# Kernel tuning notes

Hardware: AMD Instinct MI355X
Metric: run time of the kernel (lower is better)

## Reference

```python
import jax, jax.numpy as jnp
import numpy as np

EPS = 1e-5

def avg_pool3s2(x):
    # AvgPool2d(kernel=3, stride=2, no padding) on NCHW
    s = jax.lax.reduce_window(x, 0.0, jax.lax.add, (1, 1, 3, 3), (1, 1, 2, 2), 'VALID')
    return s / 9.0

def conv1x1(x, W):
    # x: [n,c,h,w], W: [out,c]
    return jnp.einsum('nchw,oc->nohw', x, W)

def batchnorm(x, g, b):
    # training-mode BN over (N,H,W), biased variance (matches torch normalization)
    m = x.mean(axis=(0, 2, 3), keepdims=True)
    v = x.var(axis=(0, 2, 3), keepdims=True)
    return (x - m) * jax.lax.rsqrt(v + EPS) * g[None, :, None, None] + b[None, :, None, None]

def coord_features(hp, wp):
    # [8, hp, wp]: xmin, ymin, xmax, ymax, xctr, yctr, 1/W, 1/H
    w = jnp.arange(wp, dtype=jnp.float32)
    h = jnp.arange(hp, dtype=jnp.float32)
    xmin = w / wp * 2 - 1
    xmax = (w + 1) / wp * 2 - 1
    xctr = (xmin + xmax) / 2
    ymin = h / hp * 2 - 1
    ymax = (h + 1) / hp * 2 - 1
    yctr = (ymin + ymax) / 2
    bx = lambda a: jnp.broadcast_to(a[None, :], (hp, wp))
    by = lambda a: jnp.broadcast_to(a[:, None], (hp, wp))
    const = lambda v: jnp.full((hp, wp), v, dtype=jnp.float32)
    return jnp.stack([bx(xmin), by(ymin), bx(xmax), by(ymax), bx(xctr), by(yctr),
                      const(1.0 / wp), const(1.0 / hp)], axis=0)

def resize_bilinear_ac(x, H, W):
    # bilinear upsample with align_corners=True, x: [n,c,h,w]
    h, w = x.shape[2], x.shape[3]
    ys = jnp.linspace(0.0, h - 1.0, H)
    xs = jnp.linspace(0.0, w - 1.0, W)
    y0 = jnp.floor(ys).astype(jnp.int32); y1 = jnp.minimum(y0 + 1, h - 1); wy = (ys - y0)[None, None, :, None]
    x0 = jnp.floor(xs).astype(jnp.int32); x1 = jnp.minimum(x0 + 1, w - 1); wx = (xs - x0)[None, None, None, :]
    rows = x[:, :, y0, :] * (1 - wy) + x[:, :, y1, :] * wy          # [n,c,H,w]
    return rows[:, :, :, x0] * (1 - wx) + rows[:, :, :, x1] * wx    # [n,c,H,W]

def setup_inputs() -> dict:
    key = jax.random.key(0)
    ks = jax.random.split(key, 8)
    n, in_dim, hid, h, w = 4, 256, 10, 129, 129
    d = hid + 8  # 18
    return {
        'p_fea': jax.random.normal(ks[0], (n, in_dim, h, w), dtype=jnp.float32),
        'hu': jax.random.normal(ks[1], (n, hid, h, w), dtype=jnp.float32),
        'Wq': jax.random.normal(ks[2], (d, d), dtype=jnp.float32) * 0.05,
        'Wk': jax.random.normal(ks[3], (d, in_dim + 8), dtype=jnp.float32) * 0.05,
        'Wv': jax.random.normal(ks[4], (128, in_dim), dtype=jnp.float32) * 0.05,
        'g_v': jnp.ones((128,), dtype=jnp.float32),
        'b_v': jnp.zeros((128,), dtype=jnp.float32),
        'Wp': jax.random.normal(ks[5], (hid, 128), dtype=jnp.float32) * 0.05,
        'g_p': jnp.ones((hid,), dtype=jnp.float32),
        'b_p': jnp.zeros((hid,), dtype=jnp.float32),
    }

def reference(p_fea, hu, Wq, Wk, Wv, g_v, b_v, Wp, g_p, b_p):
    n, c, h, w = p_fea.shape
    p = avg_pool3s2(p_fea)   # [n,256,hp,wp]
    u = avg_pool3s2(hu)      # [n,10,hp,wp]
    hp, wp = p.shape[2], p.shape[3]
    L = hp * wp
    coord = jnp.broadcast_to(coord_features(hp, wp)[None], (n, 8, hp, wp))
    query = conv1x1(jnp.concatenate([u, coord], axis=1), Wq).reshape(n, -1, L).transpose(0, 2, 1)  # [n,L,18]
    key_t = conv1x1(jnp.concatenate([p, coord], axis=1), Wk).reshape(n, -1, L)                      # [n,18,L]
    val = jax.nn.relu(batchnorm(conv1x1(p, Wv), g_v, b_v)).reshape(n, 128, L)                       # [n,128,L]
    energy = jnp.einsum('nlc,ncm->nlm', query, key_t)            # [n,L,L]
    attn = jax.nn.softmax(energy, axis=-1)
    ctx = jnp.einsum('ncm,nlm->ncl', val, attn).reshape(n, 128, hp, wp)
    ctx = jax.nn.relu(batchnorm(conv1x1(ctx, Wp), g_p, b_p))     # [n,10,hp,wp]
    return resize_bilinear_ac(ctx, h, w)                          # [n,10,h,w]
```

## Files before the change

kernel.cpp:

```cpp
#include <hip/hip_runtime.h>
#include <hip/hip_bf16.h>
#include <cstdint>

#define NN   4
#define LL   4096
#define DD   18
#define CVV  128
#define CIN  256
#define CUU  10
#define HH   129
#define COO  10

typedef unsigned short ushort_t;
typedef __attribute__((ext_vector_type(8))) short short8v;
typedef __attribute__((ext_vector_type(4))) float f32x4;

#define P_OFF    ((size_t)0)
#define U_OFF    ((size_t)4194304)
#define VP_OFF   ((size_t)4358144)
#define QT_OFF   ((size_t)6455296)
#define KT_OFF   ((size_t)6717440)
#define VT_OFF   ((size_t)6979584)
#define VSC_OFF  ((size_t)8028160)
#define VSH_OFF  ((size_t)8028288)
#define S2_OFF   ((size_t)8028416)
#define SH2_OFF  ((size_t)8028432)
#define PART_OFF ((size_t)8028448)
#define ML_OFF   ((size_t)8030496)

static __device__ __forceinline__ ushort_t f2bf(float x) {
    unsigned int u = __float_as_uint(x);
    unsigned int r = (u + 0x7fffu + ((u >> 16) & 1u)) >> 16;
    return (ushort_t)r;
}

static __device__ __forceinline__ void gload16(const void* g, void* l) {
    __builtin_amdgcn_global_load_lds(
        (const __attribute__((address_space(1))) void*)g,
        (__attribute__((address_space(3))) void*)l, 16, 0, 0);
}

__global__ __launch_bounds__(256) void pool2_kernel(const float* __restrict__ src,
                                                    float* __restrict__ dst) {
    int b = blockIdx.x;
    int plane = b >> 4;
    int rg = b & 15;
    __shared__ float rows[9][132];
    const float* sp = src + (size_t)plane * (HH * HH) + (size_t)(rg * 8) * HH;
    #pragma unroll
    for (int j = 0; j < 9; ++j) {
        if (threadIdx.x < HH) rows[j][threadIdx.x] = sp[(size_t)j * HH + threadIdx.x];
    }
    __syncthreads();
    int row = threadIdx.x >> 6, ow = threadIdx.x & 63;
    const float* r0 = rows[2 * row];
    const float* r1 = rows[2 * row + 1];
    const float* r2 = rows[2 * row + 2];
    int x = 2 * ow;
    float sum = r0[x] + r0[x + 1] + r0[x + 2]
              + r1[x] + r1[x + 1] + r1[x + 2]
              + r2[x] + r2[x + 1] + r2[x + 2];
    dst[(size_t)plane * 4096 + (size_t)(rg * 4 + row) * 64 + ow] = sum * (1.0f / 9.0f);
}

__global__ __launch_bounds__(256) void qk2_kernel(const float* __restrict__ p,
                                                  const float* __restrict__ u,
                                                  const float* __restrict__ Wq,
                                                  const float* __restrict__ Wk,
                                                  ushort_t* __restrict__ qt,
                                                  char* __restrict__ kt_c) {
    int n = blockIdx.x >> 6;
    int mb = blockIdx.x & 63;
    int tid = threadIdx.x;
    int mloc = tid & 63;
    int cs = tid >> 6;
    int m = mb * 64 + mloc;
    int hi = m >> 6, wi = m & 63;

    __shared__ float kacc[4][64][21];

    float coord[8];
    coord[0] = wi * (2.0f / 64.0f) - 1.0f;
    coord[1] = hi * (2.0f / 64.0f) - 1.0f;
    coord[2] = (wi + 1) * (2.0f / 64.0f) - 1.0f;
    coord[3] = (hi + 1) * (2.0f / 64.0f) - 1.0f;
    coord[4] = 0.5f * (coord[0] + coord[2]);
    coord[5] = 0.5f * (coord[1] + coord[3]);
    coord[6] = 1.0f / 64.0f;
    coord[7] = 1.0f / 64.0f;

    {
        float acc[DD];
        #pragma unroll
        for (int o = 0; o < DD; ++o) acc[o] = 0.0f;
        const float* pc = p + ((size_t)(n * CIN + cs * 64)) * LL + m;
        for (int c0 = 0; c0 < 64; ++c0) {
            float pv = pc[(size_t)c0 * LL];
            const float* wr = Wk + (cs * 64 + c0);
            #pragma unroll
            for (int o = 0; o < DD; ++o) acc[o] = fmaf(pv, wr[o * 264], acc[o]);
        }
        if (cs == 3) {
            #pragma unroll
            for (int j = 0; j < 8; ++j) {
                float cv = coord[j];
                #pragma unroll
                for (int o = 0; o < DD; ++o) acc[o] = fmaf(cv, Wk[o * 264 + CIN + j], acc[o]);
            }
        }
        #pragma unroll
        for (int o = 0; o < DD; ++o) kacc[cs][mloc][o] = acc[o];
    }
    if (cs == 0) {
        float acc[DD];
        #pragma unroll
        for (int o = 0; o < DD; ++o) acc[o] = 0.0f;
        for (int cq = 0; cq < CUU; ++cq) {
            float uv = u[((size_t)(n * CUU + cq)) * LL + m];
            #pragma unroll
            for (int o = 0; o < DD; ++o) acc[o] = fmaf(uv, Wq[o * DD + cq], acc[o]);
        }
        #pragma unroll
        for (int j = 0; j < 8; ++j) {
            float cv = coord[j];
            #pragma unroll
            for (int o = 0; o < DD; ++o) acc[o] = fmaf(cv, Wq[o * DD + CUU + j], acc[o]);
        }
        union { short8v v[4]; ushort_t s[32]; } pk;
        #pragma unroll
        for (int o = 0; o < 32; ++o) pk.s[o] = (o < DD) ? f2bf(acc[o]) : (ushort_t)0;
        short8v* qrow = (short8v*)(qt + ((size_t)(n * LL) + m) * 32);
        #pragma unroll
        for (int j = 0; j < 4; ++j) qrow[j] = pk.v[j];
    }
    __syncthreads();
    {
        int j = cs;
        union { short8v v; ushort_t s[8]; } pk;
        #pragma unroll
        for (int i = 0; i < 8; ++i) {
            int o = j * 8 + i;
            float v = 0.0f;
            if (o < DD)
                v = kacc[0][mloc][o] + kacc[1][mloc][o] + kacc[2][mloc][o] + kacc[3][mloc][o];
            pk.s[i] = (o < DD) ? f2bf(v) : (ushort_t)0;
        }
        int byte = ((mloc << 6) | (j << 4)) ^ (((mloc >> 1) & 7) << 4);
        *(short8v*)(kt_c + (size_t)n * 262144 + (size_t)mb * 4096 + byte) = pk.v;
    }
}

__global__ __launch_bounds__(256, 2) void val_gemm2_kernel(const float* __restrict__ p,
                                                           const float* __restrict__ Wv,
                                                           float* __restrict__ val_pre) {
    int b = blockIdx.x;
    int n  = b >> 7;
    int cb = (b >> 5) & 3;
    int mb = b & 31;
    int tid = threadIdx.x;
    int cg = tid >> 5;
    int mg = tid & 31;
    int ch0 = cb * 32;
    int m0 = mb * 128;

    __shared__ float Wt[256][36];

    {
        int c4 = tid & 63;
        int chq = tid >> 6;
        #pragma unroll
        for (int j = 0; j < 8; ++j) {
            int ch = chq * 8 + j;
            float4 v = *(const float4*)&Wv[(size_t)(ch0 + ch) * CIN + c4 * 4];
            Wt[c4 * 4 + 0][ch] = v.x;
            Wt[c4 * 4 + 1][ch] = v.y;
            Wt[c4 * 4 + 2][ch] = v.z;
            Wt[c4 * 4 + 3][ch] = v.w;
        }
    }
    __syncthreads();

    const float* pb = p + (size_t)n * CIN * LL + m0 + mg * 4;
    f32x4 a0 = {0.f,0.f,0.f,0.f}, a1 = {0.f,0.f,0.f,0.f};
    f32x4 a2 = {0.f,0.f,0.f,0.f}, a3 = {0.f,0.f,0.f,0.f};

    #pragma unroll 4
    for (int c = 0; c < CIN; ++c) {
        f32x4 pv = *(const f32x4*)(pb + (size_t)c * LL);
        f32x4 wv = *(const f32x4*)&Wt[c][cg * 4];
        a0 += pv * wv.x;
        a1 += pv * wv.y;
        a2 += pv * wv.z;
        a3 += pv * wv.w;
    }

    size_t out = ((size_t)(n * CVV + ch0 + cg * 4)) * LL + m0 + mg * 4;
    *(f32x4*)&val_pre[out]           = a0;
    *(f32x4*)&val_pre[out + LL]      = a1;
    *(f32x4*)&val_pre[out + 2 * LL]  = a2;
    *(f32x4*)&val_pre[out + 3 * LL]  = a3;
}

__global__ __launch_bounds__(256) void bn_partial_kernel(const float* __restrict__ src,
                                                         float* __restrict__ part, int C) {
    int ch = blockIdx.x >> 3;
    int s = blockIdx.x & 7;
    float s1 = 0.0f, s2 = 0.0f;
    #pragma unroll
    for (int k = 0; k < 8; ++k) {
        int e = s * 2048 + k * 256 + threadIdx.x;
        int n = e >> 12;
        int m = e & 4095;
        float v = src[((size_t)(n * C + ch)) * LL + m];
        s1 += v;
        s2 = fmaf(v, v, s2);
    }
    __shared__ float rs[4], rs2[4];
    #pragma unroll
    for (int off = 32; off; off >>= 1) {
        s1 += __shfl_down(s1, off);
        s2 += __shfl_down(s2, off);
    }
    int wid = threadIdx.x >> 6;
    if ((threadIdx.x & 63) == 0) { rs[wid] = s1; rs2[wid] = s2; }
    __syncthreads();
    if (threadIdx.x == 0) {
        part[(size_t)blockIdx.x * 2]     = rs[0] + rs[1] + rs[2] + rs[3];
        part[(size_t)blockIdx.x * 2 + 1] = rs2[0] + rs2[1] + rs2[2] + rs2[3];
    }
}

__global__ __launch_bounds__(128) void bn_finalize_kernel(const float* __restrict__ part,
                                                          const float* __restrict__ g,
                                                          const float* __restrict__ bta,
                                                          float* __restrict__ scale,
                                                          float* __restrict__ shift, int C) {
    int ch = threadIdx.x;
    if (ch >= C) return;
    float s1 = 0.0f, s2 = 0.0f;
    #pragma unroll
    for (int s = 0; s < 8; ++s) {
        s1 += part[(size_t)(ch * 8 + s) * 2];
        s2 += part[(size_t)(ch * 8 + s) * 2 + 1];
    }
    float mean = s1 * (1.0f / (NN * LL));
    float var = s2 * (1.0f / (NN * LL)) - mean * mean;
    float inv = rsqrtf(var + 1e-5f);
    float sc = g[ch] * inv;
    scale[ch] = sc;
    shift[ch] = bta[ch] - mean * sc;
}

__global__ __launch_bounds__(256) void bn_apply_kernel(const float* __restrict__ val_pre,
                                                       const float* __restrict__ scale,
                                                       const float* __restrict__ shift,
                                                       char* __restrict__ vt_c) {
    int t = blockIdx.x * 256 + threadIdx.x;
    int m = t & 4095;
    int ch = (t >> 12) & 127;
    int n = t >> 19;
    float v = val_pre[((size_t)(n * CVV + ch)) * LL + m];
    v = fmaf(v, scale[ch], shift[ch]);
    ushort_t r = f2bf(fmaxf(v, 0.0f));
    int tile = m >> 6, mloc = m & 63;
    size_t byte = (size_t)n * 1048576 + (size_t)tile * 16384
                + (size_t)(((ch << 7) | (mloc << 1)) ^ ((ch & 7) << 4));
    *(ushort_t*)(vt_c + byte) = r;
}

struct PW { union { ushort_t p[16][72]; float ot[16][20]; }; };

__global__ __launch_bounds__(256, 2) void attn_flash_kernel(const ushort_t* __restrict__ qt,
                                                            const char* __restrict__ kt_c,
                                                            const char* __restrict__ vt_c,
                                                            float* __restrict__ Op,
                                                            float* __restrict__ Mp,
                                                            float* __restrict__ Lp) {
    int orig = blockIdx.x;
    int bid = ((orig & 7) << 6) | (orig >> 3);
    int qb = bid & 63;
    int sM = (bid >> 6) & 1;
    int n = bid >> 7;
    int tid = threadIdx.x;
    int w = tid >> 6, lane = tid & 63, c = lane & 15, g = lane >> 4;
    int l0w = qb * 64 + w * 16;

    __shared__ __align__(16) ushort_t K_t[2][2048];
    __shared__ __align__(16) ushort_t V_t[2][8192];
    __shared__ PW pws[4];

    const char* ktb = kt_c + (size_t)n * 262144;
    const char* vtb = vt_c + (size_t)n * 1048576;
    int tk64 = sM * 32;

    short8v qf = *(const short8v*)(qt + (((size_t)n * LL + l0w + c) << 5) + g * 8);
    int vxor = (c & 7) << 4;

    float M[4] = {-3.0e38f, -3.0e38f, -3.0e38f, -3.0e38f};
    {
        const char* src = ktb + (size_t)tk64 * 4096 + w * 2048 + lane * 16;
        gload16(src, (char*)V_t[0] + w * 2048);
        gload16(src + 1024, (char*)V_t[0] + w * 2048 + 1024);
    }
    __syncthreads();
    int buf = 0;
    for (int mt = 0; mt < 16; ++mt) {
        if (mt + 1 < 16) {
            const char* src = ktb + (size_t)(tk64 + (mt + 1) * 2) * 4096 + w * 2048 + lane * 16;
            gload16(src, (char*)V_t[buf ^ 1] + w * 2048);
            gload16(src + 1024, (char*)V_t[buf ^ 1] + w * 2048 + 1024);
        }
        const char* kb = (const char*)V_t[buf];
        #pragma unroll
        for (int t = 0; t < 8; ++t) {
            int krow = t * 16 + c;
            int kby = ((krow << 6) | (g << 4)) ^ (((krow >> 1) & 7) << 4);
            short8v kf = *(const short8v*)(kb + kby);
            f32x4 S = __builtin_amdgcn_mfma_f32_16x16x32_bf16(qf, kf, (f32x4){0.f, 0.f, 0.f, 0.f}, 0, 0, 0);
            #pragma unroll
            for (int r = 0; r < 4; ++r) M[r] = fmaxf(M[r], S[r]);
        }
        __syncthreads();
        buf ^= 1;
    }
    #pragma unroll
    for (int off = 1; off < 16; off <<= 1) {
        #pragma unroll
        for (int r = 0; r < 4; ++r) M[r] = fmaxf(M[r], __shfl_xor(M[r], off));
    }

    f32x4 O[8];
    #pragma unroll
    for (int i = 0; i < 8; ++i) O[i] = (f32x4){0.f, 0.f, 0.f, 0.f};
    float Lacc[4] = {0.f, 0.f, 0.f, 0.f};

    {
        const char* ks = ktb + (size_t)tk64 * 4096 + w * 1024 + lane * 16;
        gload16(ks, (char*)K_t[0] + w * 1024);
        const char* vs = vtb + (size_t)tk64 * 16384 + w * 4096 + lane * 16;
        #pragma unroll
        for (int i = 0; i < 4; ++i)
            gload16(vs + i * 1024, (char*)V_t[0] + w * 4096 + i * 1024);
    }
    __syncthreads();
    buf = 0;
    for (int mt = 0; mt < 32; ++mt) {
        if (mt + 1 < 32) {
            const char* ks = ktb + (size_t)(tk64 + mt + 1) * 4096 + w * 1024 + lane * 16;
            gload16(ks, (char*)K_t[buf ^ 1] + w * 1024);
            const char* vs = vtb + (size_t)(tk64 + mt + 1) * 16384 + w * 4096 + lane * 16;
            #pragma unroll
            for (int i = 0; i < 4; ++i)
                gload16(vs + i * 1024, (char*)V_t[buf ^ 1] + w * 4096 + i * 1024);
        }
        f32x4 S[4];
        const char* kb = (const char*)K_t[buf];
        #pragma unroll
        for (int t = 0; t < 4; ++t) {
            int krow = t * 16 + c;
            int kby = ((krow << 6) | (g << 4)) ^ (((krow >> 1) & 7) << 4);
            short8v kf = *(const short8v*)(kb + kby);
            S[t] = __builtin_amdgcn_mfma_f32_16x16x32_bf16(qf, kf, (f32x4){0.f, 0.f, 0.f, 0.f}, 0, 0, 0);
        }
        #pragma unroll
        for (int t = 0; t < 4; ++t) {
            #pragma unroll
            for (int r = 0; r < 4; ++r) {
                float pv = __expf(S[t][r] - M[r]);
                Lacc[r] += pv;
                pws[w].p[g * 4 + r][t * 16 + c] = f2bf(pv);
            }
        }
        short8v pa0 = *(const short8v*)&pws[w].p[c][g * 8];
        short8v pa1 = *(const short8v*)&pws[w].p[c][32 + g * 8];
        const char* vb = (const char*)V_t[buf];
        #pragma unroll
        for (int ct = 0; ct < 8; ++ct) {
            int row = ct * 16 + c;
            int vby0 = (row << 7) | ((g << 4) ^ vxor);
            int vby1 = (row << 7) | (((1 << 6) | (g << 4)) ^ vxor);
            short8v v0 = *(const short8v*)(vb + vby0);
            short8v v1 = *(const short8v*)(vb + vby1);
            O[ct] = __builtin_amdgcn_mfma_f32_16x16x32_bf16(pa0, v0, O[ct], 0, 0, 0);
            O[ct] = __builtin_amdgcn_mfma_f32_16x16x32_bf16(pa1, v1, O[ct], 0, 0, 0);
        }
        __syncthreads();
        buf ^= 1;
    }
    #pragma unroll
    for (int off = 1; off < 16; off <<= 1) {
        #pragma unroll
        for (int r = 0; r < 4; ++r) Lacc[r] += __shfl_xor(Lacc[r], off);
    }

    size_t obase = ((size_t)(sM * NN + n) * LL + l0w);
    #pragma unroll
    for (int ct = 0; ct < 8; ++ct) {
        #pragma unroll
        for (int r = 0; r < 4; ++r) pws[w].ot[g * 4 + r][c] = O[ct][r];
        float4 v = *(float4*)&pws[w].ot[c][g * 4];
        *(float4*)&Op[(obase + c) * CVV + ct * 16 + g * 4] = v;
    }
    if (c == 0) {
        #pragma unroll
        for (int r = 0; r < 4; ++r) {
            Mp[sM * (NN * LL) + n * LL + l0w + g * 4 + r] = M[r];
            Lp[sM * (NN * LL) + n * LL + l0w + g * 4 + r] = Lacc[r];
        }
    }
}

__global__ __launch_bounds__(256) void proj_merge_kernel(const float* __restrict__ Op,
                                                         const float* __restrict__ Mp,
                                                         const float* __restrict__ Lp,
                                                         const float* __restrict__ Wp,
                                                         float* __restrict__ out_pre) {
    int idx = blockIdx.x * 256 + threadIdx.x;
    int n = idx >> 12;
    int l = idx & 4095;
    int nl = n * LL + l;
    float m0 = Mp[nl], m1 = Mp[NN * LL + nl];
    float l0v = Lp[nl], l1v = Lp[NN * LL + nl];
    float Ms = fmaxf(m0, m1);
    float w0 = __expf(m0 - Ms), w1 = __expf(m1 - Ms);
    float inv = 1.0f / (w0 * l0v + w1 * l1v);
    w0 *= inv; w1 *= inv;

    const float4* a4 = (const float4*)(Op + (size_t)nl * CVV);
    const float4* b4 = (const float4*)(Op + ((size_t)(NN * LL) + nl) * CVV);
    float acc[COO];
    #pragma unroll
    for (int o = 0; o < COO; ++o) acc[o] = 0.0f;
    for (int c4 = 0; c4 < CVV / 4; ++c4) {
        float4 a = a4[c4], b = b4[c4];
        float4 v;
        v.x = fmaf(w1, b.x, w0 * a.x);
        v.y = fmaf(w1, b.y, w0 * a.y);
        v.z = fmaf(w1, b.z, w0 * a.z);
        v.w = fmaf(w1, b.w, w0 * a.w);
        #pragma unroll
        for (int o = 0; o < COO; ++o) {
            const float* wr = Wp + o * CVV + c4 * 4;
            acc[o] = fmaf(v.x, wr[0], acc[o]);
            acc[o] = fmaf(v.y, wr[1], acc[o]);
            acc[o] = fmaf(v.z, wr[2], acc[o]);
            acc[o] = fmaf(v.w, wr[3], acc[o]);
        }
    }
    #pragma unroll
    for (int o = 0; o < COO; ++o)
        out_pre[((size_t)(n * COO + o)) * LL + l] = acc[o];
}

__global__ __launch_bounds__(256) void resize_kernel(const float* __restrict__ out_pre,
                                                     const float* __restrict__ scale,
                                                     const float* __restrict__ shift,
                                                     float* __restrict__ out,
                                                     int total) {
    int idx = blockIdx.x * 256 + threadIdx.x;
    if (idx >= total) return;
    int ow = idx % HH;
    int t = idx / HH;
    int oh = t % HH;
    int t2 = t / HH;
    int o = t2 % COO;
    int n = t2 / COO;

    const float r = 63.0f / 128.0f;
    float y = oh * r;
    float x = ow * r;
    int y0 = (int)y;
    int x0 = (int)x;
    float wy = y - y0;
    float wx = x - x0;
    int y1 = min(y0 + 1, 63);
    int x1 = min(x0 + 1, 63);

    const float* base = out_pre + ((size_t)(n * COO + o)) * LL;
    float sc = scale[o], sh = shift[o];
    float v00 = fmaxf(fmaf(base[y0 * 64 + x0], sc, sh), 0.0f);
    float v01 = fmaxf(fmaf(base[y0 * 64 + x1], sc, sh), 0.0f);
    float v10 = fmaxf(fmaf(base[y1 * 64 + x0], sc, sh), 0.0f);
    float v11 = fmaxf(fmaf(base[y1 * 64 + x1], sc, sh), 0.0f);
    float top = v00 * (1.0f - wx) + v01 * wx;
    float bot = v10 * (1.0f - wx) + v11 * wx;
    out[idx] = top * (1.0f - wy) + bot * wy;
}

extern "C" void kernel_launch(void* const* d_in, const int* in_sizes, int n_in,
                              void* d_out, int out_size, void* d_ws, size_t ws_size,
                              hipStream_t stream) {
    (void)in_sizes; (void)n_in; (void)out_size; (void)ws_size;
    const float* p_fea = (const float*)d_in[0];
    const float* hu    = (const float*)d_in[1];
    const float* Wq    = (const float*)d_in[2];
    const float* Wk    = (const float*)d_in[3];
    const float* Wv    = (const float*)d_in[4];
    const float* g_v   = (const float*)d_in[5];
    const float* b_v   = (const float*)d_in[6];
    const float* Wp    = (const float*)d_in[7];
    const float* g_p   = (const float*)d_in[8];
    const float* b_p   = (const float*)d_in[9];

    float* ws = (float*)d_ws;
    float*    p       = ws + P_OFF;
    float*    u       = ws + U_OFF;
    float*    val_pre = ws + VP_OFF;
    ushort_t* qtb     = (ushort_t*)(ws + QT_OFF);
    char*     ktb     = (char*)(ws + KT_OFF);
    char*     vtb     = (char*)(ws + VT_OFF);
    float*    Opart   = ws + P_OFF;
    float*    out_pre = ws + U_OFF;
    float*    vscale  = ws + VSC_OFF;
    float*    vshift  = ws + VSH_OFF;
    float*    scale2  = ws + S2_OFF;
    float*    shift2  = ws + SH2_OFF;
    float*    part    = ws + PART_OFF;
    float*    Mpart   = ws + ML_OFF;
    float*    Lpart   = ws + ML_OFF + 32768;

    pool2_kernel<<<NN * CIN * 16, 256, 0, stream>>>(p_fea, p);
    pool2_kernel<<<NN * CUU * 16, 256, 0, stream>>>(hu, u);
    qk2_kernel<<<256, 256, 0, stream>>>(p, u, Wq, Wk, qtb, ktb);
    val_gemm2_kernel<<<512, 256, 0, stream>>>(p, Wv, val_pre);
    bn_partial_kernel<<<CVV * 8, 256, 0, stream>>>(val_pre, part, CVV);
    bn_finalize_kernel<<<1, 128, 0, stream>>>(part, g_v, b_v, vscale, vshift, CVV);
    bn_apply_kernel<<<(NN * CVV * LL) / 256, 256, 0, stream>>>(val_pre, vscale, vshift, vtb);
    attn_flash_kernel<<<512, 256, 0, stream>>>(qtb, ktb, vtb, Opart, Mpart, Lpart);
    proj_merge_kernel<<<(NN * LL) / 256, 256, 0, stream>>>(Opart, Mpart, Lpart, Wp, out_pre);
    bn_partial_kernel<<<COO * 8, 256, 0, stream>>>(out_pre, part, COO);
    bn_finalize_kernel<<<1, 128, 0, stream>>>(part, g_p, b_p, scale2, shift2, COO);
    {
        int total = NN * COO * HH * HH;
        resize_kernel<<<(total + 255) / 256, 256, 0, stream>>>(out_pre, scale2, shift2,
                                                               (float*)d_out, total);
    }
}
```

Measured before the change: 155.1 us.

## Replace exact row-max pass with Cauchy-style bound from per-channel key abs maxima

Drops the first full QK^T pass in the attention kernel, which only computed exact row maxima. Instead, the qk kernel atomically records the per-batch, per-channel maximum absolute key value, and the attention kernel uses sum_i |q_i|*max|k_i| as an upper bound for the softmax max. The bound is shared across the two split halves, so the merge stays consistent. This halves the QK MFMA work and its K loads, but a loose bound risks exp underflow and lost precision. The BN partial and apply kernels are also vectorised to 8 elements per thread with float4 loads and 16-byte packed bf16 stores.

```diff
diff --git a/kernel.cpp b/kernel.cpp
--- a/kernel.cpp
+++ b/kernel.cpp
@@ -26,7 +26,7 @@
 #define S2_OFF   ((size_t)8028416)
 #define SH2_OFF  ((size_t)8028432)
 #define PART_OFF ((size_t)8028448)
-#define ML_OFF   ((size_t)8030496)
+#define KMAX_OFF ((size_t)8030496)
 
 static __device__ __forceinline__ ushort_t f2bf(float x) {
     unsigned int u = __float_as_uint(x);
@@ -41,7 +41,9 @@
 }
 
 __global__ __launch_bounds__(256) void pool2_kernel(const float* __restrict__ src,
-                                                    float* __restrict__ dst) {
+                                                    float* __restrict__ dst,
+                                                    int* __restrict__ kz) {
+    if (kz != nullptr && blockIdx.x == 0 && threadIdx.x < 128) kz[threadIdx.x] = 0;
     int b = blockIdx.x;
     int plane = b >> 4;
     int rg = b & 15;
@@ -68,7 +70,8 @@
                                                   const float* __restrict__ Wq,
                                                   const float* __restrict__ Wk,
                                                   ushort_t* __restrict__ qt,
-                                                  char* __restrict__ kt_c) {
+                                                  char* __restrict__ kt_c,
+                                                  int* __restrict__ kmaxb) {
     int n = blockIdx.x >> 6;
     int mb = blockIdx.x & 63;
     int tid = threadIdx.x;
@@ -147,6 +150,23 @@
         }
         int byte = ((mloc << 6) | (j << 4)) ^ (((mloc >> 1) & 7) << 4);
         *(short8v*)(kt_c + (size_t)n * 262144 + (size_t)mb * 4096 + byte) = pk.v;
+
+        int mb8[8];
+        #pragma unroll
+        for (int i = 0; i < 8; ++i) mb8[i] = (int)(pk.s[i] & 0x7fffu);
+        #pragma unroll
+        for (int off = 1; off < 64; off <<= 1) {
+            #pragma unroll
+            for (int i = 0; i < 8; ++i) {
+                int ov = __shfl_xor(mb8[i], off);
+                mb8[i] = max(mb8[i], ov);
+            }
+        }
+        if (mloc == 0) {
+            #pragma unroll
+            for (int i = 0; i < 8; ++i)
+                atomicMax(&kmaxb[n * 32 + cs * 8 + i], mb8[i] << 16);
+        }
     }
 }
 
@@ -205,16 +225,15 @@
                                                          float* __restrict__ part, int C) {
     int ch = blockIdx.x >> 3;
     int s = blockIdx.x & 7;
-    float s1 = 0.0f, s2 = 0.0f;
-    #pragma unroll
-    for (int k = 0; k < 8; ++k) {
-        int e = s * 2048 + k * 256 + threadIdx.x;
-        int n = e >> 12;
-        int m = e & 4095;
-        float v = src[((size_t)(n * C + ch)) * LL + m];
-        s1 += v;
-        s2 = fmaf(v, v, s2);
-    }
+    int n = s >> 1;
+    int m0 = (s & 1) * 2048 + threadIdx.x * 8;
+    const float* b = src + ((size_t)(n * C + ch)) * LL + m0;
+    float4 a = *(const float4*)b;
+    float4 d = *(const float4*)(b + 4);
+    float s1 = a.x + a.y + a.z + a.w + d.x + d.y + d.z + d.w;
+    float s2 = a.x*a.x + a.y*a.y + a.z*a.z + a.w*a.w
+             + d.x*d.x + d.y*d.y + d.z*d.z + d.w*d.w;
+
     __shared__ float rs[4], rs2[4];
     #pragma unroll
     for (int off = 32; off; off >>= 1) {
@@ -256,26 +275,38 @@
                                                        const float* __restrict__ shift,
                                                        char* __restrict__ vt_c) {
     int t = blockIdx.x * 256 + threadIdx.x;
-    int m = t & 4095;
-    int ch = (t >> 12) & 127;
-    int n = t >> 19;
-    float v = val_pre[((size_t)(n * CVV + ch)) * LL + m];
-    v = fmaf(v, scale[ch], shift[ch]);
-    ushort_t r = f2bf(fmaxf(v, 0.0f));
-    int tile = m >> 6, mloc = m & 63;
+    int mq = t & 511;
+    int ch = (t >> 9) & 127;
+    int n = t >> 16;
+    int m0 = mq * 8;
+    const float* b = val_pre + ((size_t)(n * CVV + ch)) * LL + m0;
+    float4 a = *(const float4*)b;
+    float4 d = *(const float4*)(b + 4);
+    float sc = scale[ch], sh = shift[ch];
+    union { short8v v; ushort_t s[8]; } pk;
+    pk.s[0] = f2bf(fmaxf(fmaf(a.x, sc, sh), 0.0f));
+    pk.s[1] = f2bf(fmaxf(fmaf(a.y, sc, sh), 0.0f));
+    pk.s[2] = f2bf(fmaxf(fmaf(a.z, sc, sh), 0.0f));
+    pk.s[3] = f2bf(fmaxf(fmaf(a.w, sc, sh), 0.0f));
+    pk.s[4] = f2bf(fmaxf(fmaf(d.x, sc, sh), 0.0f));
+    pk.s[5] = f2bf(fmaxf(fmaf(d.y, sc, sh), 0.0f));
+    pk.s[6] = f2bf(fmaxf(fmaf(d.z, sc, sh), 0.0f));
+    pk.s[7] = f2bf(fmaxf(fmaf(d.w, sc, sh), 0.0f));
+    int tile = m0 >> 6, mloc = m0 & 63;
     size_t byte = (size_t)n * 1048576 + (size_t)tile * 16384
                 + (size_t)(((ch << 7) | (mloc << 1)) ^ ((ch & 7) << 4));
-    *(ushort_t*)(vt_c + byte) = r;
+    *(short8v*)(vt_c + byte) = pk.v;
 }
 
 struct PW { union { ushort_t p[16][72]; float ot[16][20]; }; };
 
-__global__ __launch_bounds__(256, 2) void attn_flash_kernel(const ushort_t* __restrict__ qt,
-                                                            const char* __restrict__ kt_c,
-                                                            const char* __restrict__ vt_c,
-                                                            float* __restrict__ Op,
-                                                            float* __restrict__ Mp,
-                                                            float* __restrict__ Lp) {
+__global__ __launch_bounds__(256, 2) void attn_flash4_kernel(const ushort_t* __restrict__ qt,
+                                                             const char* __restrict__ kt_c,
+                                                             const char* __restrict__ vt_c,
+                                                             const int* __restrict__ kmaxb,
+                                                             float* __restrict__ Op,
+                                                             float* __restrict__ Mp,
+                                                             float* __restrict__ Lp) {
     int orig = blockIdx.x;
     int bid = ((orig & 7) << 6) | (orig >> 3);
     int qb = bid & 63;
@@ -296,38 +327,21 @@
     short8v qf = *(const short8v*)(qt + (((size_t)n * LL + l0w + c) << 5) + g * 8);
     int vxor = (c & 7) << 4;
 
-    float M[4] = {-3.0e38f, -3.0e38f, -3.0e38f, -3.0e38f};
+    float bound = 0.0f;
     {
-        const char* src = ktb + (size_t)tk64 * 4096 + w * 2048 + lane * 16;
-        gload16(src, (char*)V_t[0] + w * 2048);
-        gload16(src + 1024, (char*)V_t[0] + w * 2048 + 1024);
-    }
-    __syncthreads();
-    int buf = 0;
-    for (int mt = 0; mt < 16; ++mt) {
-        if (mt + 1 < 16) {
-            const char* src = ktb + (size_t)(tk64 + (mt + 1) * 2) * 4096 + w * 2048 + lane * 16;
-            gload16(src, (char*)V_t[buf ^ 1] + w * 2048);
-            gload16(src + 1024, (char*)V_t[buf ^ 1] + w * 2048 + 1024);
-        }
-        const char* kb = (const char*)V_t[buf];
-        #pragma unroll
-        for (int t = 0; t < 8; ++t) {
-            int krow = t * 16 + c;
-            int kby = ((krow << 6) | (g << 4)) ^ (((krow >> 1) & 7) << 4);
-            short8v kf = *(const short8v*)(kb + kby);
-            f32x4 S = __builtin_amdgcn_mfma_f32_16x16x32_bf16(qf, kf, (f32x4){0.f, 0.f, 0.f, 0.f}, 0, 0, 0);
-            #pragma unroll
-            for (int r = 0; r < 4; ++r) M[r] = fmaxf(M[r], S[r]);
-        }
-        __syncthreads();
-        buf ^= 1;
-    }
-    #pragma unroll
-    for (int off = 1; off < 16; off <<= 1) {
-        #pragma unroll
-        for (int r = 0; r < 4; ++r) M[r] = fmaxf(M[r], __shfl_xor(M[r], off));
-    }
+        const int* km = kmaxb + n * 32 + g * 8;
+        #pragma unroll
+        for (int i = 0; i < 8; ++i) {
+            float kv = __int_as_float(km[i]);
+            float aq = __uint_as_float(((unsigned int)((ushort_t)qf[i]) & 0x7fffu) << 16);
+            bound = fmaf(aq, kv, bound);
+        }
+        bound += __shfl_xor(bound, 16);
+        bound += __shfl_xor(bound, 32);
+    }
+    float M[4];
+    #pragma unroll
+    for (int r = 0; r < 4; ++r) M[r] = __shfl(bound, g * 4 + r);
 
     f32x4 O[8];
     #pragma unroll
@@ -343,7 +357,7 @@
             gload16(vs + i * 1024, (char*)V_t[0] + w * 4096 + i * 1024);
     }
     __syncthreads();
-    buf = 0;
+    int buf = 0;
     for (int mt = 0; mt < 32; ++mt) {
         if (mt + 1 < 32) {
             const char* ks = ktb + (size_t)(tk64 + mt + 1) * 4096 + w * 1024 + lane * 16;
@@ -404,8 +418,9 @@
     if (c == 0) {
         #pragma unroll
         for (int r = 0; r < 4; ++r) {
-            Mp[sM * (NN * LL) + n * LL + l0w + g * 4 + r] = M[r];
-            Lp[sM * (NN * LL) + n * LL + l0w + g * 4 + r] = Lacc[r];
+            int row = l0w + g * 4 + r;
+            Mp[sM * (NN * LL) + n * LL + row] = M[r];
+            Lp[sM * (NN * LL) + n * LL + row] = Lacc[r];
         }
     }
 }
@@ -511,22 +526,23 @@
     char*     vtb     = (char*)(ws + VT_OFF);
     float*    Opart   = ws + P_OFF;
     float*    out_pre = ws + U_OFF;
+    float*    Mpart   = ws + VP_OFF;
+    float*    Lpart   = ws + VP_OFF + 2 * 16384;
     float*    vscale  = ws + VSC_OFF;
     float*    vshift  = ws + VSH_OFF;
     float*    scale2  = ws + S2_OFF;
     float*    shift2  = ws + SH2_OFF;
     float*    part    = ws + PART_OFF;
-    float*    Mpart   = ws + ML_OFF;
-    float*    Lpart   = ws + ML_OFF + 32768;
-
-    pool2_kernel<<<NN * CIN * 16, 256, 0, stream>>>(p_fea, p);
-    pool2_kernel<<<NN * CUU * 16, 256, 0, stream>>>(hu, u);
-    qk2_kernel<<<256, 256, 0, stream>>>(p, u, Wq, Wk, qtb, ktb);
+    int*      kmaxb   = (int*)(ws + KMAX_OFF);
+
+    pool2_kernel<<<NN * CIN * 16, 256, 0, stream>>>(p_fea, p, kmaxb);
+    pool2_kernel<<<NN * CUU * 16, 256, 0, stream>>>(hu, u, nullptr);
+    qk2_kernel<<<256, 256, 0, stream>>>(p, u, Wq, Wk, qtb, ktb, kmaxb);
     val_gemm2_kernel<<<512, 256, 0, stream>>>(p, Wv, val_pre);
     bn_partial_kernel<<<CVV * 8, 256, 0, stream>>>(val_pre, part, CVV);
     bn_finalize_kernel<<<1, 128, 0, stream>>>(part, g_v, b_v, vscale, vshift, CVV);
-    bn_apply_kernel<<<(NN * CVV * LL) / 256, 256, 0, stream>>>(val_pre, vscale, vshift, vtb);
-    attn_flash_kernel<<<512, 256, 0, stream>>>(qtb, ktb, vtb, Opart, Mpart, Lpart);
+    bn_apply_kernel<<<(NN * CVV * 512) / 256, 256, 0, stream>>>(val_pre, vscale, vshift, vtb);
+    attn_flash4_kernel<<<512, 256, 0, stream>>>(qtb, ktb, vtb, kmaxb, Opart, Mpart, Lpart);
     proj_merge_kernel<<<(NN * LL) / 256, 256, 0, stream>>>(Opart, Mpart, Lpart, Wp, out_pre);
     bn_partial_kernel<<<COO * 8, 256, 0, stream>>>(out_pre, part, COO);
     bn_finalize_kernel<<<1, 128, 0, stream>>>(part, g_p, b_p, scale2, shift2, COO);
```

Result: slower. 168.0 us (+8.3%).
